# Optimization experiments

Hardware: AMD Instinct MI355X
Metric: run time of the kernel (lower is better)

## Reference

```python
import jax, jax.numpy as jnp
import numpy as np
from jax import lax

CONF_BIT = 8        # mantissa bits for block-floating-point
CONF_GROUP_SIZE = 36  # elements sharing one exponent


def bfp_quantize(x, bits=CONF_BIT, group_size=CONF_GROUP_SIZE):
    """Group-wise block-floating-point quantization (make_groups_tensor).
    Consecutive groups of `group_size` elements of the flattened tensor share
    the exponent of the group's max magnitude; mantissas are rounded to `bits` bits."""
    shape = x.shape
    flat = x.reshape(-1)
    n = flat.shape[0]
    pad = (-n) % group_size
    flat = jnp.pad(flat, (0, pad))
    g = flat.reshape(-1, group_size)
    max_abs = jnp.max(jnp.abs(g), axis=1, keepdims=True)
    # shared exponent = floor(log2(max|x|)); guard zero groups
    exp = jnp.floor(jnp.log2(jnp.where(max_abs > 0, max_abs, 1.0)))
    step = jnp.exp2(exp - (bits - 1))  # quantization step per group
    qmax = 2 ** (bits - 1) - 1
    q = jnp.clip(jnp.round(g / step), -(qmax + 1), qmax) * step
    q = jnp.where(max_abs > 0, q, 0.0)
    return q.reshape(-1)[:n].reshape(shape)


def setup_inputs() -> dict:
    key = jax.random.key(0)
    k1, k2, k3 = jax.random.split(key, 3)
    B, Cin, Cout, H, W, K = 32, 128, 128, 112, 112, 3
    x = jax.random.normal(k1, (B, Cin, H, W), dtype=jnp.float32)
    fan_in = Cin * K * K
    weight = jax.random.normal(k2, (Cout, Cin, K, K), dtype=jnp.float32) / np.sqrt(fan_in)
    bound = 1.0 / np.sqrt(fan_in)
    bias = jax.random.uniform(k3, (Cout,), dtype=jnp.float32, minval=-bound, maxval=bound)
    return {"x": x, "weight": weight, "bias": bias}


def reference(x, weight, bias):
    # BFP-quantize input and weight, then plain conv2d (stride=1, padding=1)
    xq = bfp_quantize(x)
    wq = bfp_quantize(weight)
    out = lax.conv_general_dilated(
        xq, wq,
        window_strides=(1, 1),
        padding=((1, 1), (1, 1)),
        dimension_numbers=("NCHW", "OIHW", "NCHW"),
    )
    return out + bias[None, :, None, None]
```

## Files before the change

kernel.cpp:

```cpp
#include <hip/hip_runtime.h>

typedef __attribute__((ext_vector_type(8))) short short8;
typedef __attribute__((ext_vector_type(4))) float f32x4;

#define NB     32
#define NC     128
#define HW     112
#define PLANE  12544
#define XTOT   51380224
#define NGX    1427229
#define PADW   114
#define PADPLANE 12996
#define XPAD_BYTES 106463232ULL
#define WG_OFF     XPAD_BYTES
#define SE_OFF     (XPAD_BYTES + 294912ULL)

__device__ __forceinline__ void gld_lds16(const void* g, void* l) {
  __builtin_amdgcn_global_load_lds(
      (__attribute__((address_space(1))) unsigned int*)g,
      (__attribute__((address_space(3))) unsigned int*)l, 16, 0, 0);
}

__device__ __forceinline__ float qmax4(float4 v, float m) {
  m = fmaxf(m, fabsf(v.x)); m = fmaxf(m, fabsf(v.y));
  m = fmaxf(m, fabsf(v.z)); m = fmaxf(m, fabsf(v.w));
  return m;
}

__device__ __forceinline__ int bfp_exp(float m) {
  int e = 0;
  if (m > 0.f) {
    e = (int)((__float_as_uint(m) >> 23) & 255) - 127;
    if (e < -100) e = -100;
  }
  return e;
}

__device__ __forceinline__ unsigned short bfp_q(float v, float inv, float st) {
  float qq = fminf(fmaxf(rintf(v * inv), -128.f), 127.f) * st;
  return (unsigned short)(__float_as_uint(qq) >> 16);
}

__device__ __forceinline__ float mk_inv(int e) {
  return __uint_as_float((unsigned)(134 - e) << 23);
}
__device__ __forceinline__ float mk_st(int e) {
  return __uint_as_float((unsigned)(120 + e) << 23);
}

__global__ __launch_bounds__(256) void quant_step_x(const float* __restrict__ x,
                                                    signed char* __restrict__ se) {
  __shared__ float lds[9216];
  const int t = threadIdx.x;
  const int base = blockIdx.x * 9216;
  const float4* src = (const float4*)(x + base);
  const int rem4 = (XTOT - base) >> 2;
#pragma unroll
  for (int j = 0; j < 9; ++j) {
    int idx = j * 256 + t;
    float4 v = make_float4(0.f, 0.f, 0.f, 0.f);
    if (idx < rem4) v = src[idx];
    ((float4*)lds)[idx] = v;
  }
  __syncthreads();
  int g = blockIdx.x * 256 + t;
  if (g >= NGX) return;
  const float4* p4 = (const float4*)(lds + t * 36);
  float m = 0.f;
#pragma unroll
  for (int j = 0; j < 9; ++j) m = qmax4(p4[j], m);
  se[g] = (signed char)bfp_exp(m);
}

__global__ __launch_bounds__(256) void quant_w_kernel(const float* __restrict__ w,
                                                      unsigned short* __restrict__ wg) {
  __shared__ float wl[9216];
  __shared__ float wi[256], wsr[256];
  const int blk = blockIdx.x;
  const int t = threadIdx.x;
  const int base = blk * 9216;
  const float4* src = (const float4*)(w + base);
#pragma unroll
  for (int j = 0; j < 9; ++j) ((float4*)wl)[j * 256 + t] = src[j * 256 + t];
  __syncthreads();
  {
    const float4* p4 = (const float4*)(wl + t * 36);
    float m = 0.f;
#pragma unroll
    for (int j = 0; j < 9; ++j) m = qmax4(p4[j], m);
    int e = bfp_exp(m);
    wi[t] = mk_inv(e); wsr[t] = mk_st(e);
  }
  __syncthreads();
  const int cloc = t >> 5, cil = t & 31;
  const int co = blk * 8 + cloc;
#pragma unroll
  for (int stp = 0; stp < 36; ++stp) {
    int cib = stp & 3, rs = stp >> 2;
    int ci = cib * 32 + cil;
    int fl = cloc * 1152 + ci * 9 + rs;
    int g = fl / 36;
    wg[(stp * 128 + co) * 32 + cil] = bfp_q(wl[fl], wi[g], wsr[g]);
  }
}

#define TSTR 136
__global__ __launch_bounds__(256) void quant_pad_x(const float* __restrict__ x,
                                                   const signed char* __restrict__ se,
                                                   unsigned short* __restrict__ xpad) {
  __shared__ unsigned short tile[32 * TSTR];
  __shared__ float4 ist4[128];
  __shared__ unsigned char roll[128];
  int b = blockIdx.y;
  int p0 = blockIdx.x * 32;
  int t = threadIdx.x;

  int hid = (blockIdx.y * 392 + blockIdx.x) * 256 + t;
  if (hid < NB * 452 * 16) {
    int hb = hid / (452 * 16);
    int r = hid % (452 * 16);
    int pos = r >> 4, cc = r & 15;
    int hp, wp;
    if (pos < 114)      { hp = 0;             wp = pos; }
    else if (pos < 228) { hp = 113;           wp = pos - 114; }
    else if (pos < 340) { hp = pos - 228 + 1; wp = 0; }
    else                { hp = pos - 340 + 1; wp = 113; }
    float4 z = make_float4(0.f, 0.f, 0.f, 0.f);
    *(float4*)&xpad[((size_t)((hb * 114 + hp) * 114 + wp)) * 128 + cc * 8] = z;
  }

  if (t < 128) {
    int ci = t;
    int f0 = (b * 128 + ci) * PLANE + p0;
    int g = f0 / 36;
    int rem = f0 - g * 36;
    roll[ci] = (unsigned char)(36 - rem);
    int g1 = g + 1; if (g1 > NGX - 1) g1 = NGX - 1;
    int e0 = se[g], e1 = se[g1];
    ist4[ci] = make_float4(mk_inv(e0), mk_st(e0), mk_inv(e1), mk_st(e1));
  }
  __syncthreads();

  int pq  = (t & 7) * 4;
  int ci0 = (t >> 3) * 4;
  unsigned short q[4][4];
#pragma unroll
  for (int i = 0; i < 4; ++i) {
    int ci = ci0 + i;
    int f = (b * 128 + ci) * PLANE + p0 + pq;
    float4 v = *(const float4*)(x + f);
    float vv[4] = {v.x, v.y, v.z, v.w};
    float4 is_ = ist4[ci];
    int rl = roll[ci];
#pragma unroll
    for (int j = 0; j < 4; ++j) {
      bool sec = (pq + j) >= rl;
      float inv = sec ? is_.z : is_.x;
      float st  = sec ? is_.w : is_.y;
      q[i][j] = bfp_q(vv[j], inv, st);
    }
  }
#pragma unroll
  for (int j = 0; j < 4; ++j)
    *(ushort4*)&tile[(pq + j) * TSTR + ci0] = make_ushort4(q[0][j], q[1][j], q[2][j], q[3][j]);
  __syncthreads();
  int pl = t >> 3;
  int cc = t & 7;
  int p = p0 + pl;
  int h = p / 112, w = p % 112;
  float4 v0 = *(const float4*)&tile[pl * TSTR + cc * 16];
  float4 v1 = *(const float4*)&tile[pl * TSTR + cc * 16 + 8];
  size_t dst = ((size_t)((b * 114 + h + 1) * 114 + (w + 1))) * 128 + cc * 16;
  *(float4*)&xpad[dst]     = v0;
  *(float4*)&xpad[dst + 8] = v1;
}

#define BUFSZ 16384
#define WB4() asm volatile("s_waitcnt vmcnt(4)\n\ts_barrier" ::: "memory")
#define WB0() asm volatile("s_waitcnt vmcnt(0)\n\ts_barrier" ::: "memory")

__global__ __launch_bounds__(256) void conv_mfma(const unsigned short* __restrict__ xpad,
                                                 const unsigned short* __restrict__ wg,
                                                 const float* __restrict__ bias,
                                                 float* __restrict__ out) {
  __shared__ __align__(16) char smb[3 * BUFSZ];
  const int t = threadIdx.x;
  const int lane = t & 63, wv = t >> 6;
  const int lane15 = lane & 15, quad = lane >> 4;
  const int wm = wv >> 1, wn = wv & 1;
  const int b = blockIdx.y;
  const int p0 = blockIdx.x * 128;

  int a_src[2], b_src[2];
#pragma unroll
  for (int i = 0; i < 2; ++i) {
    int idx = t + i * 256;
    int row = idx >> 2;
    int c = idx & 3;
    int sw = (row >> 1) & 3;
    a_src[i] = row * 32 + (c ^ sw) * 8;
    int p = p0 + row;
    int h = p / 112, ww = p % 112;
    b_src[i] = ((b * 114 + h) * 114 + ww) * 128 + (c ^ sw) * 8;
  }

  int a_off[4], b_off[4];
#pragma unroll
  for (int f = 0; f < 4; ++f) {
    int row = wm * 64 + f * 16 + lane15;
    a_off[f] = row * 64 + ((quad ^ ((row >> 1) & 3)) * 16);
    int prow = wn * 64 + f * 16 + lane15;
    b_off[f] = 8192 + prow * 64 + ((quad ^ ((prow >> 1) & 3)) * 16);
  }

  f32x4 acc[4][4];
  f32x4 zero = {0.f, 0.f, 0.f, 0.f};
#pragma unroll
  for (int i = 0; i < 4; ++i)
#pragma unroll
    for (int j = 0; j < 4; ++j) acc[i][j] = zero;

  auto stage = [&](int step, char* dst) {
    int rs = step >> 2, cib = step & 3;
    int r = (rs * 11) >> 5;
    int s = rs - r * 3;
    int aofs = step * 4096;
    int bofs = (r * 114 + s) * 128 + cib * 32;
#pragma unroll
    for (int i = 0; i < 2; ++i) {
      gld_lds16(wg + aofs + a_src[i],   dst + wv * 1024 + i * 4096);
      gld_lds16(xpad + b_src[i] + bofs, dst + 8192 + wv * 1024 + i * 4096);
    }
  };

  auto compute = [&](const char* sb) {
    short8 af[4], bf[4];
#pragma unroll
    for (int f = 0; f < 4; ++f) af[f] = *(const short8*)(sb + a_off[f]);
#pragma unroll
    for (int f = 0; f < 4; ++f) bf[f] = *(const short8*)(sb + b_off[f]);
    __builtin_amdgcn_s_setprio(1);
#pragma unroll
    for (int i = 0; i < 4; ++i)
#pragma unroll
      for (int j = 0; j < 4; ++j)
        acc[i][j] = __builtin_amdgcn_mfma_f32_16x16x32_bf16(af[i], bf[j], acc[i][j], 0, 0, 0);
    __builtin_amdgcn_s_setprio(0);
  };

  char* B0 = smb;
  char* B1 = smb + BUFSZ;
  char* B2 = smb + 2 * BUFSZ;

  stage(0, B0);
  stage(1, B1);
#pragma unroll 1
  for (int tt = 0; tt < 33; tt += 3) {
    WB4(); stage(tt + 2, B2); compute(B0);
    WB4(); stage(tt + 3, B0); compute(B1);
    WB4(); stage(tt + 4, B1); compute(B2);
  }
  WB4(); stage(35, B2); compute(B0);
  WB4(); compute(B1);
  WB0(); compute(B2);

#pragma unroll
  for (int i = 0; i < 4; ++i)
#pragma unroll
    for (int j = 0; j < 4; ++j) {
      int p = p0 + wn * 64 + j * 16 + lane15;
#pragma unroll
      for (int rr = 0; rr < 4; ++rr) {
        int co = wm * 64 + i * 16 + quad * 4 + rr;
        out[(b * 128 + co) * PLANE + p] = acc[i][j][rr] + bias[co];
      }
    }
}

extern "C" void kernel_launch(void* const* d_in, const int* in_sizes, int n_in,
                              void* d_out, int out_size, void* d_ws, size_t ws_size,
                              hipStream_t stream) {
  const float* x    = (const float*)d_in[0];
  const float* w    = (const float*)d_in[1];
  const float* bias = (const float*)d_in[2];
  float* out = (float*)d_out;
  char* ws = (char*)d_ws;
  unsigned short* xpad = (unsigned short*)ws;
  unsigned short* wg   = (unsigned short*)(ws + WG_OFF);
  signed char*    se   = (signed char*)(ws + SE_OFF);

  quant_step_x<<<(NGX + 255) / 256, 256, 0, stream>>>(x, se);
  quant_w_kernel<<<16, 256, 0, stream>>>(w, wg);
  quant_pad_x<<<dim3(392, 32), 256, 0, stream>>>(x, se, xpad);
  conv_mfma<<<dim3(98, 32), 256, 0, stream>>>(xpad, wg, bias, out);
}
```

Before: 517.7 us.

## Load weight fragments directly into registers and shrink LDS staging to input only

Weight (A) fragments now come straight from global memory into a double-buffered register array instead of being staged through LDS. Only the padded input tile goes through LDS, so each triple-buffered LDS stage drops from 16KB to 8KB and total shared memory is halved. The K loop is fully unrolled with a single vmcnt(2) wait per step. This removes LDS write and read traffic for weights and may allow more resident blocks. In exchange, each wave issues extra global loads, weight rows are fetched redundantly by the two wn waves, and code size and register pressure grow from the full unroll.

```diff
diff --git a/kernel.cpp b/kernel.cpp
--- a/kernel.cpp
+++ b/kernel.cpp
@@ -175,15 +175,11 @@
   *(float4*)&xpad[dst + 8] = v1;
 }
 
-#define BUFSZ 16384
-#define WB4() asm volatile("s_waitcnt vmcnt(4)\n\ts_barrier" ::: "memory")
-#define WB0() asm volatile("s_waitcnt vmcnt(0)\n\ts_barrier" ::: "memory")
-
 __global__ __launch_bounds__(256) void conv_mfma(const unsigned short* __restrict__ xpad,
                                                  const unsigned short* __restrict__ wg,
                                                  const float* __restrict__ bias,
                                                  float* __restrict__ out) {
-  __shared__ __align__(16) char smb[3 * BUFSZ];
+  __shared__ __align__(16) char smb[3 * 8192];
   const int t = threadIdx.x;
   const int lane = t & 63, wv = t >> 6;
   const int lane15 = lane & 15, quad = lane >> 4;
@@ -191,27 +187,29 @@
   const int b = blockIdx.y;
   const int p0 = blockIdx.x * 128;
 
-  int a_src[2], b_src[2];
+  int b_src[2];
 #pragma unroll
   for (int i = 0; i < 2; ++i) {
     int idx = t + i * 256;
     int row = idx >> 2;
     int c = idx & 3;
     int sw = (row >> 1) & 3;
-    a_src[i] = row * 32 + (c ^ sw) * 8;
     int p = p0 + row;
     int h = p / 112, ww = p % 112;
     b_src[i] = ((b * 114 + h) * 114 + ww) * 128 + (c ^ sw) * 8;
   }
 
-  int a_off[4], b_off[4];
+  int b_off[4];
 #pragma unroll
   for (int f = 0; f < 4; ++f) {
-    int row = wm * 64 + f * 16 + lane15;
-    a_off[f] = row * 64 + ((quad ^ ((row >> 1) & 3)) * 16);
     int prow = wn * 64 + f * 16 + lane15;
-    b_off[f] = 8192 + prow * 64 + ((quad ^ ((prow >> 1) & 3)) * 16);
-  }
+    b_off[f] = prow * 64 + ((quad ^ ((prow >> 1) & 3)) * 16);
+  }
+
+  int a_goff[4];
+#pragma unroll
+  for (int f = 0; f < 4; ++f)
+    a_goff[f] = (wm * 64 + f * 16 + lane15) * 32 + quad * 8;
 
   f32x4 acc[4][4];
   f32x4 zero = {0.f, 0.f, 0.f, 0.f};
@@ -224,19 +222,20 @@
     int rs = step >> 2, cib = step & 3;
     int r = (rs * 11) >> 5;
     int s = rs - r * 3;
-    int aofs = step * 4096;
     int bofs = (r * 114 + s) * 128 + cib * 32;
 #pragma unroll
-    for (int i = 0; i < 2; ++i) {
-      gld_lds16(wg + aofs + a_src[i],   dst + wv * 1024 + i * 4096);
-      gld_lds16(xpad + b_src[i] + bofs, dst + 8192 + wv * 1024 + i * 4096);
-    }
+    for (int i = 0; i < 2; ++i)
+      gld_lds16(xpad + b_src[i] + bofs, dst + wv * 1024 + i * 4096);
   };
 
-  auto compute = [&](const char* sb) {
-    short8 af[4], bf[4];
-#pragma unroll
-    for (int f = 0; f < 4; ++f) af[f] = *(const short8*)(sb + a_off[f]);
+  auto loadA = [&](int step, short8* ar) {
+    const unsigned short* wp_ = wg + step * 4096;
+#pragma unroll
+    for (int f = 0; f < 4; ++f) ar[f] = *(const short8*)(wp_ + a_goff[f]);
+  };
+
+  auto compute = [&](const char* sb, const short8* ar) {
+    short8 bf[4];
 #pragma unroll
     for (int f = 0; f < 4; ++f) bf[f] = *(const short8*)(sb + b_off[f]);
     __builtin_amdgcn_s_setprio(1);
@@ -244,25 +243,22 @@
     for (int i = 0; i < 4; ++i)
 #pragma unroll
       for (int j = 0; j < 4; ++j)
-        acc[i][j] = __builtin_amdgcn_mfma_f32_16x16x32_bf16(af[i], bf[j], acc[i][j], 0, 0, 0);
+        acc[i][j] = __builtin_amdgcn_mfma_f32_16x16x32_bf16(ar[i], bf[j], acc[i][j], 0, 0, 0);
     __builtin_amdgcn_s_setprio(0);
   };
 
-  char* B0 = smb;
-  char* B1 = smb + BUFSZ;
-  char* B2 = smb + 2 * BUFSZ;
-
-  stage(0, B0);
-  stage(1, B1);
-#pragma unroll 1
-  for (int tt = 0; tt < 33; tt += 3) {
-    WB4(); stage(tt + 2, B2); compute(B0);
-    WB4(); stage(tt + 3, B0); compute(B1);
-    WB4(); stage(tt + 4, B1); compute(B2);
-  }
-  WB4(); stage(35, B2); compute(B0);
-  WB4(); compute(B1);
-  WB0(); compute(B2);
+  short8 areg[2][4];
+  loadA(0, areg[0]);
+  stage(0, smb);
+  stage(1, smb + 8192);
+
+#pragma unroll
+  for (int T = 0; T < 36; ++T) {
+    asm volatile("s_waitcnt vmcnt(2)\n\ts_barrier" ::: "memory");
+    loadA(T + 1 < 36 ? T + 1 : 35, areg[(T + 1) & 1]);
+    stage(T + 2 < 36 ? T + 2 : 35, smb + ((T + 2) % 3) * 8192);
+    compute(smb + (T % 3) * 8192, areg[T & 1]);
+  }
 
 #pragma unroll
   for (int i = 0; i < 4; ++i)
```

New measurement: 558.1 us. 7.8% more time.
